# Optimization experiments

Hardware: AMD Instinct MI355X
Metric: run time of the kernel (lower is better)

## Reference

```python
import jax, jax.numpy as jnp
import numpy as np

B, L, IN_DIM, D, H = 4, 1024, 256, 512, 8
DH = D // H
LARGE_NEG = -10000.0
LN_EPS = 1e-5


def _layernorm(x, g, b):
    mu = jnp.mean(x, axis=-1, keepdims=True)
    var = jnp.mean((x - mu) ** 2, axis=-1, keepdims=True)
    return (x - mu) * jax.lax.rsqrt(var + LN_EPS) * g + b


def setup_inputs() -> dict:
    key = jax.random.key(0)
    ks = jax.random.split(key, 16)
    s = 0.02
    return {
        "x": jax.random.normal(ks[0], (B, L, IN_DIM), jnp.float32),
        "attention_mask": jax.random.bernoulli(ks[1], 0.5, (B, L, L)),
        "adjacency_matrix": jax.random.uniform(ks[2], (B, L, L), jnp.float32),
        "W_fuse": jax.random.normal(ks[3], (D, IN_DIM), jnp.float32) * s,
        "b_fuse": jnp.zeros((D,), jnp.float32),
        "in_proj_w": jax.random.normal(ks[4], (3 * D, D), jnp.float32) * s,
        "in_proj_b": jnp.zeros((3 * D,), jnp.float32),
        "out_w": jax.random.normal(ks[5], (D, D), jnp.float32) * s,
        "out_b": jnp.zeros((D,), jnp.float32),
        "ln1_g": jnp.ones((D,), jnp.float32),
        "ln1_b": jnp.zeros((D,), jnp.float32),
        "ln2_g": jnp.ones((D,), jnp.float32),
        "ln2_b": jnp.zeros((D,), jnp.float32),
        "W1": jax.random.normal(ks[6], (4 * D, D), jnp.float32) * s,
        "b1": jnp.zeros((4 * D,), jnp.float32),
        "W2": jax.random.normal(ks[7], (D, 4 * D), jnp.float32) * s,
        "b2": jnp.zeros((D,), jnp.float32),
        "log_scale": jnp.array(0.0, jnp.float32),  # log(adj_bias_strength=1.0)
    }


def reference(x, attention_mask, adjacency_matrix, W_fuse, b_fuse, in_proj_w,
              in_proj_b, out_w, out_b, ln1_g, ln1_b, ln2_g, ln2_b,
              W1, b1, W2, b2, log_scale):
    # fuse projection (in_dim != d_model)
    x = jnp.einsum("bli,di->bld", x, W_fuse) + b_fuse

    # ensure_self_loops_in_mask: unmask diagonal of fully-masked rows
    eye = jnp.eye(L, dtype=bool)
    row_all = jnp.all(attention_mask, axis=-1)  # [B, L]
    mask = attention_mask & ~(eye[None, :, :] & row_all[:, :, None])

    # additive attention bias: large_neg where masked + scaled clipped adjacency
    bias = jnp.where(mask, LARGE_NEG, 0.0) + \
        jnp.exp(log_scale) * jnp.clip(adjacency_matrix, 0.0, 1.0)  # [B, L, L]

    # --- attention block (pre-norm) ---
    x_norm = _layernorm(x, ln1_g, ln1_b)
    qkv = jnp.einsum("bld,ed->ble", x_norm, in_proj_w) + in_proj_b
    q, k, v = jnp.split(qkv, 3, axis=-1)
    q = q.reshape(B, L, H, DH).transpose(0, 2, 1, 3)  # [B,H,L,DH]
    k = k.reshape(B, L, H, DH).transpose(0, 2, 1, 3)
    v = v.reshape(B, L, H, DH).transpose(0, 2, 1, 3)
    scores = jnp.einsum("bhqd,bhkd->bhqk", q, k) / np.sqrt(DH) + bias[:, None]
    probs = jax.nn.softmax(scores, axis=-1)
    ctx = jnp.einsum("bhqk,bhkd->bhqd", probs, v)
    ctx = ctx.transpose(0, 2, 1, 3).reshape(B, L, D)
    attn_out = jnp.einsum("bld,ed->ble", ctx, out_w) + out_b
    x = x + attn_out

    # --- FFN block (pre-norm) ---
    x_norm = _layernorm(x, ln2_g, ln2_b)
    h = jax.nn.gelu(jnp.einsum("bld,fd->blf", x_norm, W1) + b1, approximate=False)
    ff = jnp.einsum("blf,df->bld", h, W2) + b2
    return x + ff
```

## Files before the change

### kernel.cpp

```cpp
#include <hip/hip_runtime.h>
#include <math.h>

typedef unsigned short UST;
typedef __attribute__((ext_vector_type(8))) short bf16x8;
typedef __attribute__((ext_vector_type(4))) float f32x4;

#define BB 4
#define LL 1024
#define IND 256
#define DD 512
#define HH 8
#define FFD 2048
#define NT (BB*LL)

__device__ __forceinline__ float bf2f(UST u){ return __uint_as_float(((unsigned)u)<<16); }
__device__ __forceinline__ UST f2bf(float f){
  unsigned u = __float_as_uint(f);
  u += 0x7FFFu + ((u>>16)&1u);
  return (UST)(u>>16);
}
__device__ __forceinline__ float ldF(const void* p, long i, int isf32){
  return isf32 ? ((const float*)p)[i] : bf2f(((const UST*)p)[i]);
}
__device__ __forceinline__ bool ldMask(const void* p, long i, int fm){
  if (fm==0) return ((const int*)p)[i] != 0;
  if (fm==1) return ((const unsigned char*)p)[i] != 0;
  if (fm==2) return ((const UST*)p)[i] != 0;
  return ((const float*)p)[i] != 0.f;
}
__device__ __forceinline__ f32x4 mfma16(bf16x8 a, bf16x8 b, f32x4 c){
  return __builtin_amdgcn_mfma_f32_16x16x32_bf16(a, b, c, 0, 0, 0);
}
__device__ __forceinline__ void gld16(const void* g, void* l){
  __builtin_amdgcn_global_load_lds((const __attribute__((address_space(1))) unsigned int*)g,
                                   (__attribute__((address_space(3))) unsigned int*)l, 16, 0, 0);
}

__global__ void detect_k(int* flags, const UST* xh, const unsigned int* mw){
  int lane = threadIdx.x & 63;
  int e0 = (xh[lane] >> 7) & 0xFF;
  int e1 = (xh[64+lane] >> 7) & 0xFF;
  int f32 = __any((e0 >= 140) || (e1 >= 140)) ? 1 : 0;
  unsigned v = mw[lane];
  int w01   = __all(v <= 1u) ? 1 : 0;
  unsigned lo = v & 0xFFFFu, hi = v >> 16;
  int half  = __all((lo==0u||lo==0x3F80u) && (hi==0u||hi==0x3F80u)) ? 1 : 0;
  int wordF = __all(v==0u || v==0x3F800000u) ? 1 : 0;
  int byteB = __all((v & 0xFEFEFEFEu) == 0u) ? 1 : 0;
  if (lane == 0){
    flags[0] = f32;
    flags[1] = w01 ? 0 : (half ? (wordF ? 3 : 2) : (byteB ? 1 : 0));
  }
}

struct CvtArgs { const void* src[11]; UST* dst[11]; int n[11]; };
__global__ __launch_bounds__(256) void prep_k(const int* flags, CvtArgs a,
    const void* mask, const void* adj, const void* lsp, UST* biasOut){
  int bid = blockIdx.x;
  int t = threadIdx.x;
  if (bid < BB*LL){
    int fF = flags[0], fM = flags[1];
    int row = bid;
    int i = row & (LL-1);
    long base = (long)row * LL;
    int j0 = t*4;
    bool mv[4];
    if (fM == 0){
      int4 m4 = *(const int4*)((const int*)mask + base + j0);
      mv[0]=m4.x!=0; mv[1]=m4.y!=0; mv[2]=m4.z!=0; mv[3]=m4.w!=0;
    } else {
      #pragma unroll
      for (int k=0;k<4;++k) mv[k] = ldMask(mask, base + j0 + k, fM);
    }
    float a4[4];
    if (fF){
      float4 av = *(const float4*)((const float*)adj + base + j0);
      a4[0]=av.x; a4[1]=av.y; a4[2]=av.z; a4[3]=av.w;
    } else {
      const UST* ap = (const UST*)adj + base + j0;
      #pragma unroll
      for (int k=0;k<4;++k) a4[k] = bf2f(ap[k]);
    }
    int my = (mv[0]&&mv[1]&&mv[2]&&mv[3]) ? 1 : 0;
    int wa = __all(my);
    __shared__ int sAll[4];
    int w = t >> 6;
    if ((t & 63) == 0) sAll[w] = wa;
    __syncthreads();
    int rowAll = sAll[0] & sAll[1] & sAll[2] & sAll[3];
    float es = expf(ldF(lsp, 0, fF));
    UST o4[4];
    #pragma unroll
    for (int k = 0; k < 4; ++k){
      int j = j0 + k;
      float av = fminf(fmaxf(a4[k], 0.f), 1.f);
      bool eff = mv[k] && !((rowAll != 0) && (j == i));
      o4[k] = f2bf(((eff ? -10000.f : 0.f) + es * av) * 1.44269504f);
    }
    *(int2*)(biasOut + base + j0) = *(const int2*)o4;
  } else {
    int cb = bid - BB*LL;
    int ti = cb >> 9, xi = cb & 511;
    int n = a.n[ti];
    long i8 = ((long)xi*256 + t)*8;
    if (i8 >= n) return;
    const void* s = a.src[ti]; UST* d = a.dst[ti];
    if (flags[0]){
      const float4* sf = (const float4*)s;
      float4 a0 = sf[i8>>2], a1 = sf[(i8>>2)+1];
      UST o[8] = { f2bf(a0.x),f2bf(a0.y),f2bf(a0.z),f2bf(a0.w),
                   f2bf(a1.x),f2bf(a1.y),f2bf(a1.z),f2bf(a1.w) };
      *(int4*)(d+i8) = *(const int4*)o;
    } else {
      ((int4*)d)[i8>>3] = ((const int4*)s)[i8>>3];
    }
  }
}

template<int TM, int TN, int ACT, int RES, int OUTMODE>
__global__ __launch_bounds__(256) void gemm3_k(const int* flags,
    const UST* __restrict__ A, const UST* __restrict__ Bw, const UST* __restrict__ bias,
    const float* __restrict__ resid, void* Cout, int M, int N, int K){
  constexpr int MI = TM/32, NI = TN/32;
  __shared__ UST sA[2][TM*64];
  __shared__ UST sB[2][TN*64];
  int t = threadIdx.x, w = t>>6, lane = t&63, l15 = lane&15, qd = lane>>4;
  int m0 = blockIdx.x*TM, n0 = blockIdx.y*TN;
  int wm = (w&1)*(TM/2), wn = (w>>1)*(TN/2);
  f32x4 acc[MI][NI];
  #pragma unroll
  for (int mi=0; mi<MI; ++mi)
    #pragma unroll
    for (int ni=0; ni<NI; ++ni){ acc[mi][ni][0]=0;acc[mi][ni][1]=0;acc[mi][ni][2]=0;acc[mi][ni][3]=0; }
  int sRow = lane&7, sCol = (lane>>3)*8;
  const UST* aS = A + (long)(m0 + w*(TM/4) + sRow)*K + sCol;
  const UST* bS = Bw + (long)(n0 + w*(TN/4) + sRow)*K + sCol;
  auto stage = [&](int buf, int k0){
    #pragma unroll
    for (int c=0;c<MI;++c) gld16(aS + (long)c*8*K + k0, (char*)&sA[buf][(w*(TM/4)+c*8)*64]);
    #pragma unroll
    for (int c=0;c<NI;++c) gld16(bS + (long)c*8*K + k0, (char*)&sB[buf][(w*(TN/4)+c*8)*64]);
  };
  stage(0, 0);
  for (int k0 = 0; k0 < K; k0 += 64){
    int cur = (k0>>6)&1, nxt = cur^1;
    __syncthreads();
    if (k0 + 64 < K) stage(nxt, k0+64);
    #pragma unroll
    for (int ks=0; ks<2; ++ks){
      bf16x8 afr[MI], bfr[NI];
      #pragma unroll
      for (int mi=0; mi<MI; ++mi){
        int R = wm + mi*16 + l15;
        afr[mi] = *(const bf16x8*)&sA[cur][(R>>3)*512 + (ks*4+qd)*64 + (R&7)*8];
      }
      #pragma unroll
      for (int ni=0; ni<NI; ++ni){
        int R = wn + ni*16 + l15;
        bfr[ni] = *(const bf16x8*)&sB[cur][(R>>3)*512 + (ks*4+qd)*64 + (R&7)*8];
      }
      #pragma unroll
      for (int mi=0; mi<MI; ++mi)
        #pragma unroll
        for (int ni=0; ni<NI; ++ni)
          acc[mi][ni] = mfma16(afr[mi], bfr[ni], acc[mi][ni]);
    }
  }
  int outF32 = (OUTMODE==1) || (OUTMODE==2 && flags[0]);
  #pragma unroll
  for (int mi=0; mi<MI; ++mi){
    #pragma unroll
    for (int ni=0; ni<NI; ++ni){
      int gc = n0 + wn + ni*16 + l15;
      float bv = bf2f(bias[gc]);
      #pragma unroll
      for (int r=0; r<4; ++r){
        int grow = m0 + wm + mi*16 + qd*4 + r;
        float c = acc[mi][ni][r] + bv;
        if (ACT) c = 0.5f*c*(1.f+erff(c*0.70710678118654752f));
        long oi = (long)grow*N + gc;
        if (RES) c += resid[oi];
        if (outF32) ((float*)Cout)[oi] = c;
        else ((UST*)Cout)[oi] = f2bf(c);
      }
    }
  }
}

__global__ __launch_bounds__(256) void ln_k(const int* flags, const float* xin,
    const void* gp, const void* bp, UST* xout){
  int fF = flags[0];
  int row = blockIdx.x, t = threadIdx.x;
  const float* xr = xin + (long)row * DD;
  float v0 = xr[t], v1 = xr[t+256];
  float s = v0+v1, q = v0*v0 + v1*v1;
  #pragma unroll
  for (int off=1; off<64; off<<=1){ s += __shfl_xor(s,off,64); q += __shfl_xor(q,off,64); }
  __shared__ float rs[4], rq[4];
  int w = t>>6;
  if ((t&63)==0){ rs[w]=s; rq[w]=q; }
  __syncthreads();
  float S = rs[0]+rs[1]+rs[2]+rs[3];
  float Q = rq[0]+rq[1]+rq[2]+rq[3];
  float mean = S * (1.f/DD);
  float var  = fmaxf(Q * (1.f/DD) - mean*mean, 0.f);
  float ri = rsqrtf(var + 1e-5f);
  float g0 = ldF(gp, t, fF), b0 = ldF(bp, t, fF);
  float g1 = ldF(gp, t+256, fF), b1 = ldF(bp, t+256, fF);
  xout[(long)row*DD + t]     = f2bf((v0-mean)*ri*g0 + b0);
  xout[(long)row*DD + t+256] = f2bf((v1-mean)*ri*g1 + b1);
}

__global__ __launch_bounds__(256) void repack_v(const UST* __restrict__ qkv, UST* __restrict__ vT){
  int id = blockIdx.x;
  int bh = id & 31, qt = id >> 5;
  int b = bh >> 3, h = bh & 7;
  int t = threadIdx.x, w = t >> 6, lane = t & 63;
  int token = qt*64 + lane;
  const UST* src = qkv + ((long)(b*LL + token))*1536 + 1024 + h*64;
  #pragma unroll
  for (int c = 0; c < 2; ++c){
    int ch = w*2 + c;
    union { int4 v; UST u[8]; } uu;
    uu.v = *(const int4*)(src + ch*8);
    #pragma unroll
    for (int i = 0; i < 8; ++i)
      vT[((long)(bh*64 + ch*8 + i))*LL + token] = uu.u[i];
  }
}

__global__ __launch_bounds__(256) void attn_k(const UST* __restrict__ qkv,
    const UST* __restrict__ vT, const UST* __restrict__ bias, UST* __restrict__ ctx){
  int id = blockIdx.x;
  int b = id & 3, h = (id>>2) & 7, qt = id >> 5;
  int bh = b*HH + h;
  int q0 = qt*64;
  int t = threadIdx.x, w = t>>6, lane = t&63, l15 = lane&15, qd = lane>>4;
  __shared__ UST sK[2][2][64*32];
  __shared__ UST sV[2][2][64*32];
  __shared__ UST sB[2][2][64*32];
  __shared__ UST sP[4][16*72];
  UST* myP = &sP[w][0];

  const UST* qrow = qkv + ((long)(b*LL + q0 + w*16 + l15))*1536 + h*64;
  bf16x8 qf0 = *(const bf16x8*)(qrow + qd*8);
  bf16x8 qf1 = *(const bf16x8*)(qrow + 32 + qd*8);

  const UST* kS = qkv + (long)(b*LL + w*16 + (lane&15))*1536 + 512 + h*64 + (lane>>4)*8;
  const UST* vS = vT + (long)(bh*64 + w*16 + (lane&15))*LL + (lane>>4)*8;
  int rowS = t>>2, colS = (t&3)*8;
  const UST* bS = bias + ((long)b<<20) + (long)(q0 + rowS)*LL + colS;

  f32x4 o[4]; float lsum[4];
  #pragma unroll
  for (int i=0;i<4;i++){ o[i][0]=0;o[i][1]=0;o[i][2]=0;o[i][3]=0; lsum[i]=0.f; }
  const float C1 = 0.18033688f;

  auto stage = [&](int buf, int k0){
    gld16(kS + (long)k0*1536,      (char*)sK[buf][0] + w*1024);
    gld16(kS + (long)k0*1536 + 32, (char*)sK[buf][1] + w*1024);
    gld16(vS + k0,                 (char*)sV[buf][0] + w*1024);
    gld16(vS + k0 + 32,            (char*)sV[buf][1] + w*1024);
    gld16(bS + k0,                 (char*)sB[buf][0] + w*1024);
    gld16(bS + k0 + 32,            (char*)sB[buf][1] + w*1024);
  };
  stage(0, 0);

  for (int kt = 0; kt < 16; ++kt){
    int cur = kt&1, nxt = cur^1;
    int k0 = kt*64;
    __syncthreads();
    if (kt < 15) stage(nxt, k0+64);
    f32x4 s4[4];
    #pragma unroll
    for (int i=0;i<4;i++){ s4[i][0]=0;s4[i][1]=0;s4[i][2]=0;s4[i][3]=0; }
    #pragma unroll
    for (int ni=0; ni<4; ++ni){
      bf16x8 kf0 = *(const bf16x8*)&sK[cur][0][ni*512 + qd*128 + l15*8];
      bf16x8 kf1 = *(const bf16x8*)&sK[cur][1][ni*512 + qd*128 + l15*8];
      s4[ni] = mfma16(qf0, kf0, s4[ni]);
      s4[ni] = mfma16(qf1, kf1, s4[ni]);
    }
    float p[4][4];
    #pragma unroll
    for (int ni=0; ni<4; ++ni){
      const UST* sBc = sB[cur][ni>>1];
      int nc = (ni & 1)*16 + l15;
      #pragma unroll
      for (int r=0; r<4; ++r){
        float bzv = bf2f(sBc[(w*16 + qd*4 + r)*32 + nc]);
        p[ni][r] = exp2f(fmaf(s4[ni][r], C1, bzv));
      }
    }
    #pragma unroll
    for (int r=0; r<4; ++r)
      lsum[r] += (p[0][r]+p[1][r]) + (p[2][r]+p[3][r]);
    #pragma unroll
    for (int ni=0; ni<4; ++ni)
      #pragma unroll
      for (int r=0; r<4; ++r) myP[(qd*4+r)*72 + ni*16 + l15] = f2bf(p[ni][r]);
    bf16x8 pf0 = *(const bf16x8*)&myP[l15*72 + qd*8];
    bf16x8 pf1 = *(const bf16x8*)&myP[l15*72 + 32 + qd*8];
    #pragma unroll
    for (int dn=0; dn<4; ++dn){
      bf16x8 vf0 = *(const bf16x8*)&sV[cur][0][dn*512 + qd*128 + l15*8];
      bf16x8 vf1 = *(const bf16x8*)&sV[cur][1][dn*512 + qd*128 + l15*8];
      o[dn] = mfma16(pf0, vf0, o[dn]);
      o[dn] = mfma16(pf1, vf1, o[dn]);
    }
  }
  float linv[4];
  #pragma unroll
  for (int r=0; r<4; ++r){
    float s = lsum[r];
    #pragma unroll
    for (int off=1; off<16; off<<=1) s += __shfl_xor(s, off, 64);
    linv[r] = 1.f / s;
  }
  #pragma unroll
  for (int dn=0; dn<4; ++dn){
    #pragma unroll
    for (int r=0; r<4; ++r){
      long oi = ((long)(b*LL + q0 + w*16 + qd*4 + r))*DD + h*64 + dn*16 + l15;
      ctx[oi] = f2bf(o[dn][r] * linv[r]);
    }
  }
}

extern "C" void kernel_launch(void* const* d_in, const int* in_sizes, int n_in,
                              void* d_out, int out_size, void* d_ws, size_t ws_size,
                              hipStream_t stream){
  char* ws = (char*)d_ws;
  size_t o = 0;
  auto alloc = [&](size_t b){ size_t r = o; o += (b + 255) & ~(size_t)255; return r; };
  int*   flags = (int*)(ws + alloc(256));
  size_t biasOff = alloc(8UL<<20);
  size_t qkvOff  = alloc(12UL<<20);
  UST* biasC = (UST*)(ws + biasOff);
  UST* qkv   = (UST*)(ws + qkvOff);
  UST* hb    = (UST*)(ws + biasOff);
  UST* vT    = (UST*)(ws + alloc(4UL<<20));
  UST* xbf   = (UST*)(ws + alloc(2UL<<20));
  UST* wfuse = (UST*)(ws + alloc(131072*2));
  UST* bfuse = (UST*)(ws + alloc(1024));
  UST* ipw   = (UST*)(ws + alloc(786432*2));
  UST* ipb   = (UST*)(ws + alloc(3072*2));
  UST* outw  = (UST*)(ws + alloc(262144*2));
  UST* outb  = (UST*)(ws + alloc(1024));
  UST* w1    = (UST*)(ws + alloc(1048576*2));
  UST* b1    = (UST*)(ws + alloc(4096*2));
  UST* w2    = (UST*)(ws + alloc(1048576*2));
  UST* b2    = (UST*)(ws + alloc(1024));
  float* xf  = (float*)(ws + alloc((size_t)NT*DD*4));
  UST* xn    = (UST*)(ws + alloc((size_t)NT*DD*2));
  UST* ctx   = (UST*)(ws + alloc((size_t)NT*DD*2));
  float* x2  = (float*)(ws + alloc((size_t)NT*DD*4));

  detect_k<<<1, 64, 0, stream>>>(flags, (const UST*)d_in[0], (const unsigned int*)d_in[1]);

  CvtArgs ca;
  const int srcIdx[11] = {0,3,4,5,6,7,8,13,14,15,16};
  UST* dsts[11] = {xbf,wfuse,bfuse,ipw,ipb,outw,outb,w1,b1,w2,b2};
  const int ns[11] = {NT*IND, DD*IND, DD, 3*DD*DD, 3*DD, DD*DD, DD, FFD*DD, FFD, DD*FFD, DD};
  for (int i=0;i<11;i++){ ca.src[i]=d_in[srcIdx[i]]; ca.dst[i]=dsts[i]; ca.n[i]=ns[i]; }
  prep_k<<<BB*LL + 11*512, 256, 0, stream>>>(flags, ca, d_in[1], d_in[2], d_in[17], biasC);

  gemm3_k<64,64,0,0,1><<<dim3(64,8), 256, 0, stream>>>(flags, xbf, wfuse, bfuse, nullptr, xf, NT, DD, IND);
  ln_k<<<NT, 256, 0, stream>>>(flags, xf, d_in[9], d_in[10], xn);
  gemm3_k<64,128,0,0,0><<<dim3(64,12), 256, 0, stream>>>(flags, xn, ipw, ipb, nullptr, qkv, NT, 3*DD, DD);
  repack_v<<<512, 256, 0, stream>>>(qkv, vT);
  attn_k<<<512, 256, 0, stream>>>(qkv, vT, biasC, ctx);
  gemm3_k<64,64,0,1,1><<<dim3(64,8), 256, 0, stream>>>(flags, ctx, outw, outb, xf, x2, NT, DD, DD);
  ln_k<<<NT, 256, 0, stream>>>(flags, x2, d_in[11], d_in[12], xn);
  gemm3_k<64,128,1,0,0><<<dim3(64,16), 256, 0, stream>>>(flags, xn, w1, b1, nullptr, hb, NT, FFD, DD);
  gemm3_k<64,64,0,1,2><<<dim3(64,8), 256, 0, stream>>>(flags, hb, w2, b2, x2, d_out, NT, DD, FFD);
}
```

Before: 279.6 us.

## Split-K the FFN down-projection with a reduction kernel and enlarge FFN tiles

Gives the GEMM template a K-slice parameter and a partial-output mode. The W2 GEMM (K=2048) now runs as four K-splits on 128x128 tiles, each writing fp32 partial sums to workspace. A separate reduction kernel then adds the partials, bias and residual. The W1 GEMM also moves to 128x128 tiles. The aim is more data reuse per tile and enough blocks to fill the GPU on the long-K GEMM, at the cost of 32MB of extra partial-sum traffic and one more launch.

```diff
diff --git a/kernel.cpp b/kernel.cpp
--- a/kernel.cpp
+++ b/kernel.cpp
@@ -120,12 +120,13 @@
 template<int TM, int TN, int ACT, int RES, int OUTMODE>
 __global__ __launch_bounds__(256) void gemm3_k(const int* flags,
     const UST* __restrict__ A, const UST* __restrict__ Bw, const UST* __restrict__ bias,
-    const float* __restrict__ resid, void* Cout, int M, int N, int K){
+    const float* __restrict__ resid, void* Cout, int M, int N, int K, int Ks){
   constexpr int MI = TM/32, NI = TN/32;
   __shared__ UST sA[2][TM*64];
   __shared__ UST sB[2][TN*64];
   int t = threadIdx.x, w = t>>6, lane = t&63, l15 = lane&15, qd = lane>>4;
   int m0 = blockIdx.x*TM, n0 = blockIdx.y*TN;
+  int zoff = blockIdx.z * Ks;
   int wm = (w&1)*(TM/2), wn = (w>>1)*(TN/2);
   f32x4 acc[MI][NI];
   #pragma unroll
@@ -133,8 +134,8 @@
     #pragma unroll
     for (int ni=0; ni<NI; ++ni){ acc[mi][ni][0]=0;acc[mi][ni][1]=0;acc[mi][ni][2]=0;acc[mi][ni][3]=0; }
   int sRow = lane&7, sCol = (lane>>3)*8;
-  const UST* aS = A + (long)(m0 + w*(TM/4) + sRow)*K + sCol;
-  const UST* bS = Bw + (long)(n0 + w*(TN/4) + sRow)*K + sCol;
+  const UST* aS = A + (long)(m0 + w*(TM/4) + sRow)*K + sCol + zoff;
+  const UST* bS = Bw + (long)(n0 + w*(TN/4) + sRow)*K + sCol + zoff;
   auto stage = [&](int buf, int k0){
     #pragma unroll
     for (int c=0;c<MI;++c) gld16(aS + (long)c*8*K + k0, (char*)&sA[buf][(w*(TM/4)+c*8)*64]);
@@ -142,10 +143,10 @@
     for (int c=0;c<NI;++c) gld16(bS + (long)c*8*K + k0, (char*)&sB[buf][(w*(TN/4)+c*8)*64]);
   };
   stage(0, 0);
-  for (int k0 = 0; k0 < K; k0 += 64){
+  for (int k0 = 0; k0 < Ks; k0 += 64){
     int cur = (k0>>6)&1, nxt = cur^1;
     __syncthreads();
-    if (k0 + 64 < K) stage(nxt, k0+64);
+    if (k0 + 64 < Ks) stage(nxt, k0+64);
     #pragma unroll
     for (int ks=0; ks<2; ++ks){
       bf16x8 afr[MI], bfr[NI];
@@ -165,6 +166,21 @@
         for (int ni=0; ni<NI; ++ni)
           acc[mi][ni] = mfma16(afr[mi], bfr[ni], acc[mi][ni]);
     }
+  }
+  if (OUTMODE == 3){
+    float* P = (float*)Cout + (size_t)blockIdx.z * M * N;
+    #pragma unroll
+    for (int mi=0; mi<MI; ++mi)
+      #pragma unroll
+      for (int ni=0; ni<NI; ++ni){
+        int gc = n0 + wn + ni*16 + l15;
+        #pragma unroll
+        for (int r=0; r<4; ++r){
+          int grow = m0 + wm + mi*16 + qd*4 + r;
+          P[(long)grow*N + gc] = acc[mi][ni][r];
+        }
+      }
+    return;
   }
   int outF32 = (OUTMODE==1) || (OUTMODE==2 && flags[0]);
   #pragma unroll
@@ -184,6 +200,29 @@
         else ((UST*)Cout)[oi] = f2bf(c);
       }
     }
+  }
+}
+
+__global__ __launch_bounds__(256) void reduce4_k(const int* flags,
+    const float* __restrict__ parts, const UST* __restrict__ bias,
+    const float* __restrict__ resid, void* __restrict__ dout){
+  const long S = (long)NT*DD;
+  long e = ((long)blockIdx.x*256 + threadIdx.x)*4;
+  float4 a = *(const float4*)(parts + e);
+  float4 b = *(const float4*)(parts + S + e);
+  float4 c = *(const float4*)(parts + 2*S + e);
+  float4 d = *(const float4*)(parts + 3*S + e);
+  float4 r = *(const float4*)(resid + e);
+  int gc = (int)(e & (DD-1));
+  float v[4] = { a.x+b.x+c.x+d.x + bf2f(bias[gc+0]) + r.x,
+                 a.y+b.y+c.y+d.y + bf2f(bias[gc+1]) + r.y,
+                 a.z+b.z+c.z+d.z + bf2f(bias[gc+2]) + r.z,
+                 a.w+b.w+c.w+d.w + bf2f(bias[gc+3]) + r.w };
+  if (flags[0]){
+    *(float4*)((float*)dout + e) = *(const float4*)v;
+  } else {
+    UST o4[4] = { f2bf(v[0]), f2bf(v[1]), f2bf(v[2]), f2bf(v[3]) };
+    *(int2*)((UST*)dout + e) = *(const int2*)o4;
   }
 }
 
@@ -355,6 +394,9 @@
   UST* xn    = (UST*)(ws + alloc((size_t)NT*DD*2));
   UST* ctx   = (UST*)(ws + alloc((size_t)NT*DD*2));
   float* x2  = (float*)(ws + alloc((size_t)NT*DD*4));
+  size_t partsOff = alloc(4UL*NT*DD*4);
+  float* parts = (float*)(ws + partsOff);
+  bool doSplit = (o <= ws_size);
 
   detect_k<<<1, 64, 0, stream>>>(flags, (const UST*)d_in[0], (const unsigned int*)d_in[1]);
 
@@ -365,13 +407,18 @@
   for (int i=0;i<11;i++){ ca.src[i]=d_in[srcIdx[i]]; ca.dst[i]=dsts[i]; ca.n[i]=ns[i]; }
   prep_k<<<BB*LL + 11*512, 256, 0, stream>>>(flags, ca, d_in[1], d_in[2], d_in[17], biasC);
 
-  gemm3_k<64,64,0,0,1><<<dim3(64,8), 256, 0, stream>>>(flags, xbf, wfuse, bfuse, nullptr, xf, NT, DD, IND);
+  gemm3_k<64,64,0,0,1><<<dim3(64,8), 256, 0, stream>>>(flags, xbf, wfuse, bfuse, nullptr, xf, NT, DD, IND, IND);
   ln_k<<<NT, 256, 0, stream>>>(flags, xf, d_in[9], d_in[10], xn);
-  gemm3_k<64,128,0,0,0><<<dim3(64,12), 256, 0, stream>>>(flags, xn, ipw, ipb, nullptr, qkv, NT, 3*DD, DD);
+  gemm3_k<64,128,0,0,0><<<dim3(64,12), 256, 0, stream>>>(flags, xn, ipw, ipb, nullptr, qkv, NT, 3*DD, DD, DD);
   repack_v<<<512, 256, 0, stream>>>(qkv, vT);
   attn_k<<<512, 256, 0, stream>>>(qkv, vT, biasC, ctx);
-  gemm3_k<64,64,0,1,1><<<dim3(64,8), 256, 0, stream>>>(flags, ctx, outw, outb, xf, x2, NT, DD, DD);
+  gemm3_k<64,64,0,1,1><<<dim3(64,8), 256, 0, stream>>>(flags, ctx, outw, outb, xf, x2, NT, DD, DD, DD);
   ln_k<<<NT, 256, 0, stream>>>(flags, x2, d_in[11], d_in[12], xn);
-  gemm3_k<64,128,1,0,0><<<dim3(64,16), 256, 0, stream>>>(flags, xn, w1, b1, nullptr, hb, NT, FFD, DD);
-  gemm3_k<64,64,0,1,2><<<dim3(64,8), 256, 0, stream>>>(flags, hb, w2, b2, x2, d_out, NT, DD, FFD);
-}
+  gemm3_k<128,128,1,0,0><<<dim3(32,16), 256, 0, stream>>>(flags, xn, w1, b1, nullptr, hb, NT, FFD, DD, DD);
+  if (doSplit){
+    gemm3_k<128,128,0,0,3><<<dim3(32,4,4), 256, 0, stream>>>(flags, hb, w2, b2, nullptr, parts, NT, DD, FFD, FFD/4);
+    reduce4_k<<<(NT*DD)/1024, 256, 0, stream>>>(flags, parts, b2, x2, d_out);
+  } else {
+    gemm3_k<64,64,0,1,2><<<dim3(64,8), 256, 0, stream>>>(flags, hb, w2, b2, x2, d_out, NT, DD, FFD, FFD);
+  }
+}
```

Measured after the change: 263.4 us. -5.8%, faster.
